# Kernel tuning notes

Measured on AMD Instinct MI355X. Metric: run time of the kernel, lower is better.

Reference implementation:

```python
import jax, jax.numpy as jnp
import numpy as np

N, E = 200_000, 1_000_000
WIDTH, NUM_HEAD = 128, 8
WN, WA = 1, 1            # width_norm, width_act
C = WIDTH * WN           # pre/norm channels
A = WIDTH * WA           # gate/value channels
BOND_SIZE, BAG = 33, 3
EPS = 1e-5               # GroupNorm eps (torch default)


def group_norm(x, groups, eps=EPS):
    # x: [E, C]; normalize per sample per group (affine=False, spatial size 1)
    e, c = x.shape
    xg = x.reshape(e, groups, c // groups)
    m = xg.mean(-1, keepdims=True)
    v = ((xg - m) ** 2).mean(-1, keepdims=True)
    return ((xg - m) * jax.lax.rsqrt(v + eps)).reshape(e, c)


def grouped1x1(x, w, groups):
    # grouped Conv1d with kernel 1, no bias. x: [E, Cin], w: [Cout, Cin//groups]
    e, cin = x.shape
    cout = w.shape[0]
    xg = x.reshape(e, groups, cin // groups)
    wg = w.reshape(groups, cout // groups, cin // groups)
    return jnp.einsum('egi,goi->ego', xg, wg).reshape(e, cout)


def setup_inputs() -> dict:
    key = jax.random.key(0)
    ks = jax.random.split(key, 12)
    x = jax.random.normal(ks[0], (N, WIDTH), jnp.float32)
    # degrees clamped to >= 1 in the original model
    deg = jnp.floor(jax.random.uniform(ks[1], (N,), jnp.float32, 1.0, 8.0))
    edge_idx = jax.random.randint(ks[2], (2, E), 0, N)
    edge_attr = jax.random.randint(ks[3], (E, BAG), 0, BOND_SIZE)
    s_in = 1.0 / np.sqrt(WIDTH)
    s_g = 1.0 / np.sqrt(C // NUM_HEAD)
    s_p = 1.0 / np.sqrt(A)
    pre0_w = jax.random.normal(ks[4], (C, WIDTH), jnp.float32) * s_in
    pre0_b = jnp.zeros((C,), jnp.float32)
    pre1_w = jax.random.normal(ks[5], (C, WIDTH), jnp.float32) * s_in
    pre1_b = jnp.zeros((C,), jnp.float32)
    emb = jax.random.normal(ks[6], (BOND_SIZE, C), jnp.float32)
    emb = emb.at[0].set(0.0)  # padding_idx=0
    gate_w = jax.random.normal(ks[7], (A, C // NUM_HEAD), jnp.float32) * s_g
    value_w = jax.random.normal(ks[8], (A, C // NUM_HEAD), jnp.float32) * s_g
    post_w = jax.random.normal(ks[9], (WIDTH, A), jnp.float32) * s_p
    post_b = jnp.zeros((WIDTH,), jnp.float32)
    degree_param = jnp.full((WIDTH,), -0.01, jnp.float32)
    return {"x": x, "deg": deg, "edge_idx": edge_idx, "edge_attr": edge_attr,
            "pre0_w": pre0_w, "pre0_b": pre0_b, "pre1_w": pre1_w, "pre1_b": pre1_b,
            "emb": emb, "gate_w": gate_w, "value_w": value_w,
            "post_w": post_w, "post_b": post_b, "degree_param": degree_param}


def reference(x, deg, edge_idx, edge_attr, pre0_w, pre0_b, pre1_w, pre1_b,
              emb, gate_w, value_w, post_w, post_b, degree_param):
    n = x.shape[0]
    # conv1x1 projections on nodes, then gather to edges
    h0 = x @ pre0_w.T + pre0_b                      # [N, C]
    h1 = x @ pre1_w.T + pre1_b                      # [N, C]
    xx = h0[edge_idx[0]] + h1[edge_idx[1]]          # [E, C]
    xx = group_norm(xx, NUM_HEAD)
    # EmbeddingBag mean with padding_idx=0 excluded from the mean
    mask = (edge_attr != 0)                          # [E, BAG]
    bag = (emb[edge_attr] * mask[..., None]).sum(1)  # [E, C]
    cnt = jnp.maximum(mask.sum(-1), 1).astype(xx.dtype)
    bag = bag / cnt[:, None]
    # GLU-style gate * value (Dropout is identity at eval)
    gate = jax.nn.relu(grouped1x1(xx + bag, gate_w, NUM_HEAD))  # [E, A]
    val = grouped1x1(xx, value_w, NUM_HEAD)                     # [E, A]
    xx = gate * val
    # scatter-sum back to destination nodes
    agg = jax.ops.segment_sum(xx, edge_idx[1], num_segments=n)  # [N, A]
    out = agg @ post_w.T + post_b                                # [N, WIDTH]
    out = jnp.power(deg[:, None], degree_param) * out
    return out
```

## Files before the change

kernel.cpp:

```cpp
#include <hip/hip_runtime.h>
#include <hip/hip_bf16.h>
#include <hip/hip_fp16.h>


typedef unsigned short u16;
typedef unsigned int   u32;

#define WIDTH 128

#define OFF_W0   0
#define OFF_B0   16384
#define OFF_W1   16512
#define OFF_B1   32896
#define OFF_EMB  33024
#define OFF_GW   37248
#define OFF_VW   39296
#define OFF_PW   41344
#define OFF_PB   57728
#define OFF_DP   57856
#define OFF_DEG  57984
#define ARENA_PAD 258048

typedef __attribute__((ext_vector_type(8))) short bf16x8;
typedef __attribute__((ext_vector_type(4))) float f32x4;
typedef __attribute__((ext_vector_type(2))) __fp16 f16x2;

__device__ __forceinline__ float bfl(u32 p){ return __uint_as_float(p << 16); }
__device__ __forceinline__ float bfh(u32 p){ return __uint_as_float(p & 0xffff0000u); }
__device__ __forceinline__ float b2f(u16 u){ return __uint_as_float(((u32)u) << 16); }
__device__ __forceinline__ u16   f2b(float f){
  u32 u = __float_as_uint(f);
  u += 0x7fffu + ((u >> 16) & 1u);
  return (u16)(u >> 16);
}
__device__ __forceinline__ u16   f2h(float f){ return __half_as_ushort(__float2half(f)); }

__device__ __forceinline__ f16x2 u2h(u32 u){ union { u32 a; f16x2 b; } c; c.a = u; return c.b; }
__device__ __forceinline__ u32   h2u(f16x2 h){ union { f16x2 b; u32 a; } c; c.b = h; return c.a; }

__device__ __forceinline__ float dot2h(f16x2 a, f16x2 b, float c){
#if __has_builtin(__builtin_amdgcn_fdot2)
  return __builtin_amdgcn_fdot2(a, b, c, false);
#else
  return fmaf((float)a.x, (float)b.x, fmaf((float)a.y, (float)b.y, c));
#endif
}

#define SWZF(v, imm) __uint_as_float((u32)__builtin_amdgcn_ds_swizzle((int)__float_as_uint(v), (imm)))

__device__ __forceinline__ bool is_fp32(const void* degsrc){
  return ((*(const u32*)degsrc) & 0xffffu) == 0u;
}

__device__ __forceinline__ bf16x8 cvt8(float4 a, float4 b){
  bf16x8 r;
  r[0]=(short)f2b(a.x); r[1]=(short)f2b(a.y); r[2]=(short)f2b(a.z); r[3]=(short)f2b(a.w);
  r[4]=(short)f2b(b.x); r[5]=(short)f2b(b.y); r[6]=(short)f2b(b.z); r[7]=(short)f2b(b.w);
  return r;
}

__device__ __forceinline__ u16 cvt_one(const void* src, int j, bool f32){
  return f32 ? f2b(((const float*)src)[j]) : ((const u16*)src)[j];
}
__device__ __forceinline__ u16 cvt_one_h(const void* src, int j, bool f32){
  return f32 ? f2h(((const float*)src)[j]) : f2h(b2f(((const u16*)src)[j]));
}

__global__ void k_convert(const void* w0, const void* b0, const void* w1, const void* b1,
                          const void* emb, const void* gw, const void* vw,
                          const void* pw, const void* pb, const void* dp,
                          const void* degsrc, u16* __restrict__ pb16, int total)
{
  const int i = blockIdx.x * 256 + threadIdx.x;
  if (i >= total) return;
  const bool f32 = is_fp32(degsrc);
  u16 v;
  if      (i < OFF_B0 ) v = cvt_one(w0,  i,           f32);
  else if (i < OFF_W1 ) v = cvt_one(b0,  i - OFF_B0,  f32);
  else if (i < OFF_B1 ) v = cvt_one(w1,  i - OFF_W1,  f32);
  else if (i < OFF_EMB) v = cvt_one(b1,  i - OFF_B1,  f32);
  else if (i < OFF_GW ) v = cvt_one(emb, i - OFF_EMB, f32);
  else if (i < OFF_VW ) v = cvt_one_h(gw, i - OFF_GW, f32);
  else if (i < OFF_PW ) v = cvt_one_h(vw, i - OFF_VW, f32);
  else if (i < OFF_PB ) v = cvt_one(pw,  i - OFF_PW,  f32);
  else if (i < OFF_DP ) v = cvt_one(pb,  i - OFF_PB,  f32);
  else if (i < OFF_DEG) v = cvt_one(dp,  i - OFF_DP,  f32);
  else                  v = cvt_one(degsrc, i - OFF_DEG, f32);
  pb16[i] = v;
}

__device__ __forceinline__ float read_f(const void* src, int j, bool f32){
  return f32 ? ((const float*)src)[j] : b2f(((const u16*)src)[j]);
}

__global__ void k_gemb(const void* gwsrc, const void* embsrc, const void* degsrc,
                       float* __restrict__ gemb)
{
  const int tid = blockIdx.x * 256 + threadIdx.x;
  if (tid >= 33 * 128) return;
  const bool f32 = is_fp32(degsrc);
  const int a = tid >> 7, c = tid & 127, g = c >> 4;
  float s = 0.f;
  #pragma unroll
  for (int i = 0; i < 16; ++i)
    s += read_f(gwsrc, c * 16 + i, f32) * read_f(embsrc, a * WIDTH + g * 16 + i, f32);
  gemb[tid] = s;
}

__global__ void k_zero(int* __restrict__ cnt, int n){
  const int i = blockIdx.x * 256 + threadIdx.x;
  if (i < n) cnt[i] = 0;
}

__global__ void k_hist(const int* __restrict__ eidx, int* __restrict__ cnt, int E){
  const int e = blockIdx.x * 256 + threadIdx.x;
  if (e < E) atomicAdd(&cnt[eidx[E + e]], 1);
}

__global__ void k_scan1(const int* __restrict__ cnt, int* __restrict__ bsum, int n){
  const int t = threadIdx.x, b = blockIdx.x;
  const int i0 = b * 1024 + t * 4;
  int s = 0;
  #pragma unroll
  for (int j = 0; j < 4; ++j) { int i = i0 + j; if (i < n) s += cnt[i]; }
  __shared__ int sb[256];
  sb[t] = s; __syncthreads();
  for (int d = 128; d > 0; d >>= 1) { if (t < d) sb[t] += sb[t + d]; __syncthreads(); }
  if (t == 0) bsum[b] = sb[0];
}

__global__ void k_scan2(int* __restrict__ bsum, int nblk){
  const int t = threadIdx.x;
  int v[4];
  const int i0 = t * 4;
  #pragma unroll
  for (int j = 0; j < 4; ++j) { int i = i0 + j; v[j] = (i < nblk) ? bsum[i] : 0; }
  int tsum = v[0] + v[1] + v[2] + v[3];
  __shared__ int sb[256];
  sb[t] = tsum; __syncthreads();
  for (int d = 1; d < 256; d <<= 1) {
    int x = (t >= d) ? sb[t - d] : 0;
    __syncthreads();
    sb[t] += x;
    __syncthreads();
  }
  int run = sb[t] - tsum;
  #pragma unroll
  for (int j = 0; j < 4; ++j) { int nv = run; run += v[j]; v[j] = nv; }
  #pragma unroll
  for (int j = 0; j < 4; ++j) { int i = i0 + j; if (i < nblk) bsum[i] = v[j]; }
}

__global__ void k_scan3(const int* __restrict__ cnt, const int* __restrict__ bsum,
                        int* __restrict__ off, int n){
  const int t = threadIdx.x, b = blockIdx.x;
  const int i0 = b * 1024 + t * 4;
  int c[4];
  #pragma unroll
  for (int j = 0; j < 4; ++j) { int i = i0 + j; c[j] = (i < n) ? cnt[i] : 0; }
  int tsum = c[0] + c[1] + c[2] + c[3];
  __shared__ int sb[256];
  sb[t] = tsum; __syncthreads();
  for (int d = 1; d < 256; d <<= 1) {
    int x = (t >= d) ? sb[t - d] : 0;
    __syncthreads();
    sb[t] += x;
    __syncthreads();
  }
  int run = bsum[b] + sb[t] - tsum;
  #pragma unroll
  for (int j = 0; j < 4; ++j) {
    int i = i0 + j;
    if (i < n) off[i] = run;
    run += c[j];
  }
}

__global__ void k_scatter(const int* __restrict__ eidx, const int* __restrict__ eattr,
                          int* __restrict__ off, u32* __restrict__ ssrc,
                          u32* __restrict__ sattr, int E){
  const int e = blockIdx.x * 256 + threadIdx.x;
  if (e >= E) return;
  const int dst = eidx[E + e];
  const int pos = atomicAdd(&off[dst], 1);
  ssrc[pos] = (u32)eidx[e];
  const u32 a0 = (u32)eattr[e*3+0], a1 = (u32)eattr[e*3+1], a2 = (u32)eattr[e*3+2];
  sattr[pos] = a0 | (a1 << 6) | (a2 << 12);
}

__global__ __launch_bounds__(256, 2) void k_pre(
    const void* __restrict__ x, const u16* __restrict__ pb16,
    u16* __restrict__ h0, u16* __restrict__ h1, const void* __restrict__ degsrc)
{
  const int t = threadIdx.x;
  const int lane = t & 63, lid = lane & 15, quad = lane >> 4;
  const int w = t >> 6, mat = w >> 1, c0 = (w & 1) * 64;
  const int node0 = blockIdx.x * 64;

  const u16* wm = pb16 + (mat ? OFF_W1 : OFF_W0);
  const u16* bs = pb16 + (mat ? OFF_B1 : OFF_B0);
  u16* hout = mat ? h1 : h0;
  const bool f32 = is_fp32(degsrc);

  f32x4 acc[4][4];
  #pragma unroll
  for (int nt = 0; nt < 4; ++nt) {
    const float bias = b2f(bs[c0 + nt * 16 + lid]);
    #pragma unroll
    for (int mt = 0; mt < 4; ++mt)
      #pragma unroll
      for (int r = 0; r < 4; ++r) acc[mt][nt][r] = bias;
  }

  #pragma unroll
  for (int ks = 0; ks < 4; ++ks) {
    bf16x8 a[4], b[4];
    #pragma unroll
    for (int nt = 0; nt < 4; ++nt)
      b[nt] = *(const bf16x8*)(wm + (size_t)(c0 + nt * 16 + lid) * WIDTH + ks * 32 + quad * 8);
    if (f32) {
      #pragma unroll
      for (int mt = 0; mt < 4; ++mt) {
        const float4* xr = (const float4*)((const float*)x +
            (size_t)(node0 + mt * 16 + lid) * WIDTH + ks * 32 + quad * 8);
        a[mt] = cvt8(xr[0], xr[1]);
      }
    } else {
      #pragma unroll
      for (int mt = 0; mt < 4; ++mt)
        a[mt] = *(const bf16x8*)((const u16*)x +
            (size_t)(node0 + mt * 16 + lid) * WIDTH + ks * 32 + quad * 8);
    }
    #pragma unroll
    for (int mt = 0; mt < 4; ++mt)
      #pragma unroll
      for (int nt = 0; nt < 4; ++nt)
        acc[mt][nt] = __builtin_amdgcn_mfma_f32_16x16x32_bf16(a[mt], b[nt], acc[mt][nt], 0, 0, 0);
  }

  #pragma unroll
  for (int mt = 0; mt < 4; ++mt)
    #pragma unroll
    for (int nt = 0; nt < 4; ++nt)
      #pragma unroll
      for (int r = 0; r < 4; ++r)
        hout[(size_t)(node0 + mt * 16 + quad * 4 + r) * WIDTH + c0 + nt * 16 + lid] =
            f2h(acc[mt][nt][r]);
}

__global__ __launch_bounds__(256, 4) void k_agg(
    const u16* __restrict__ h0, const u16* __restrict__ h1,
    const u32* __restrict__ ssrc, const u32* __restrict__ sattr,
    const int* __restrict__ off, const u16* __restrict__ pb16,
    const float* __restrict__ gemb, float* __restrict__ agg, const int N)
{
  const int dst = (blockIdx.x * 256 + threadIdx.x) >> 6;
  if (dst >= N) return;
  const int q = threadIdx.x & 63;
  const int c0 = 2 * q;

  u32 gw0[8], gw1[8], vw0[8], vw1[8];
  {
    const u32* g = (const u32*)(pb16 + OFF_GW + (size_t)c0 * 16);
    const u32* v = (const u32*)(pb16 + OFF_VW + (size_t)c0 * 16);
    #pragma unroll
    for (int i = 0; i < 8; ++i) {
      gw0[i] = g[i]; gw1[i] = g[8 + i];
      vw0[i] = v[i]; vw1[i] = v[8 + i];
    }
  }

  const f16x2 h1h  = u2h(*(const u32*)(h1 + (size_t)dst * WIDTH + c0));
  const f16x2 ones = u2h(0x3C003C00u);

  const int n0 = dst ? off[dst - 1] : 0;
  const int n1 = off[dst];

  float acc0 = 0.f, acc1 = 0.f;

  u32 apw = 0, hp = 0;
  if (n0 < n1) {
    const u32 s0 = ssrc[n0];
    apw = sattr[n0];
    hp  = *(const u32*)(h0 + (size_t)s0 * WIDTH + c0);
  }

  for (int i = n0; i < n1; ++i) {
    const u32 apw_c = apw, hp_c = hp;
    if (i + 1 < n1) {
      const u32 s2 = ssrc[i + 1];
      apw = sattr[i + 1];
      hp  = *(const u32*)(h0 + (size_t)s2 * WIDTH + c0);
    }

    const f16x2 xh = u2h(hp_c) + h1h;

    float s  = dot2h(xh, ones, 0.f);
    float ss = dot2h(xh, xh,   0.f);
    s  += SWZF(s,  0x041F); s  += SWZF(s,  0x081F); s  += SWZF(s,  0x101F);
    ss += SWZF(ss, 0x041F); ss += SWZF(ss, 0x081F); ss += SWZF(ss, 0x101F);
    const float mean = s * 0.0625f;
    const float var  = fmaf(ss, 0.0625f, -mean * mean);
    const float rs   = __builtin_amdgcn_rsqf(var + 1e-5f);
    const float mrs  = mean * rs;
    const float x0 = (float)xh.x, x1 = (float)xh.y;
    const f16x2 xn = __builtin_amdgcn_cvt_pkrtz(fmaf(x0, rs, -mrs), fmaf(x1, rs, -mrs));
    const u32 xnu = h2u(xn);

    const int a0 = apw_c & 63, a1 = (apw_c >> 6) & 63, a2 = (apw_c >> 12) & 63;
    const float2 g0 = *(const float2*)(gemb + (size_t)a0 * WIDTH + c0);
    const float2 g1 = *(const float2*)(gemb + (size_t)a1 * WIDTH + c0);
    const float2 g2 = *(const float2*)(gemb + (size_t)a2 * WIDTH + c0);
    const int cb = (a0 != 0) + (a1 != 0) + (a2 != 0);
    const float inv = __builtin_amdgcn_rcpf((float)(cb | (cb == 0)));

    float ga0 = (g0.x + g1.x + g2.x) * inv;
    float ga1 = (g0.y + g1.y + g2.y) * inv;
    float va0 = 0.f, va1 = 0.f;

#define CSTEP(J) {                                                             \
    const f16x2 xj = u2h((u32)__builtin_amdgcn_ds_swizzle(                     \
        (int)xnu, 0x18 | ((J) << 5)));                                         \
    ga0 = dot2h(xj, u2h(gw0[J]), ga0);                                         \
    ga1 = dot2h(xj, u2h(gw1[J]), ga1);                                         \
    va0 = dot2h(xj, u2h(vw0[J]), va0);                                         \
    va1 = dot2h(xj, u2h(vw1[J]), va1); }
    CSTEP(0) CSTEP(1) CSTEP(2) CSTEP(3) CSTEP(4) CSTEP(5) CSTEP(6) CSTEP(7)
#undef CSTEP

    acc0 = fmaf(fmaxf(ga0, 0.f), va0, acc0);
    acc1 = fmaf(fmaxf(ga1, 0.f), va1, acc1);
  }
  *(float2*)(agg + (size_t)dst * WIDTH + c0) = make_float2(acc0, acc1);
}

__global__ __launch_bounds__(256, 2) void k_post(
    const float* __restrict__ agg, const u16* __restrict__ pb16,
    void* __restrict__ out, const void* __restrict__ degsrc)
{
  const int t = threadIdx.x;
  const int lane = t & 63, lid = lane & 15, quad = lane >> 4;
  const int w = t >> 6, c0 = (w & 1) * 64, mh = (w >> 1) * 32;
  const int node0 = blockIdx.x * 64;
  const bool f32o = is_fp32(degsrc);

  f32x4 acc[2][4];
  float dpc[4];
  #pragma unroll
  for (int nt = 0; nt < 4; ++nt) {
    const float bias = b2f(pb16[OFF_PB + c0 + nt * 16 + lid]);
    dpc[nt] = b2f(pb16[OFF_DP + c0 + nt * 16 + lid]);
    #pragma unroll
    for (int mt = 0; mt < 2; ++mt)
      #pragma unroll
      for (int r = 0; r < 4; ++r) acc[mt][nt][r] = bias;
  }

  #pragma unroll
  for (int ks = 0; ks < 4; ++ks) {
    bf16x8 a[2], b[4];
    #pragma unroll
    for (int nt = 0; nt < 4; ++nt)
      b[nt] = *(const bf16x8*)(pb16 + OFF_PW + (size_t)(c0 + nt * 16 + lid) * WIDTH + ks * 32 + quad * 8);
    #pragma unroll
    for (int mt = 0; mt < 2; ++mt) {
      const float4* ar = (const float4*)(agg +
          (size_t)(node0 + mh + mt * 16 + lid) * WIDTH + ks * 32 + quad * 8);
      a[mt] = cvt8(ar[0], ar[1]);
    }
    #pragma unroll
    for (int mt = 0; mt < 2; ++mt)
      #pragma unroll
      for (int nt = 0; nt < 4; ++nt)
        acc[mt][nt] = __builtin_amdgcn_mfma_f32_16x16x32_bf16(a[mt], b[nt], acc[mt][nt], 0, 0, 0);
  }

  float logd[2][4];
  #pragma unroll
  for (int mt = 0; mt < 2; ++mt)
    #pragma unroll
    for (int r = 0; r < 4; ++r)
      logd[mt][r] = __logf(b2f(pb16[OFF_DEG + node0 + mh + mt * 16 + quad * 4 + r]));

  #pragma unroll
  for (int mt = 0; mt < 2; ++mt)
    #pragma unroll
    for (int nt = 0; nt < 4; ++nt)
      #pragma unroll
      for (int r = 0; r < 4; ++r) {
        const int node = node0 + mh + mt * 16 + quad * 4 + r;
        const float v = acc[mt][nt][r] * __expf(dpc[nt] * logd[mt][r]);
        if (f32o) ((float*)out)[(size_t)node * WIDTH + c0 + nt * 16 + lid] = v;
        else      ((u16*)out)[(size_t)node * WIDTH + c0 + nt * 16 + lid] = f2b(v);
      }
}

extern "C" void kernel_launch(void* const* d_in, const int* in_sizes, int n_in,
                              void* d_out, int out_size, void* d_ws, size_t ws_size,
                              hipStream_t stream)
{
  (void)n_in; (void)out_size; (void)ws_size;
  const void* x     = d_in[0];
  const void* deg   = d_in[1];
  const int*  eidx  = (const int*)d_in[2];
  const int*  eattr = (const int*)d_in[3];

  const int N = in_sizes[1];
  const int E = in_sizes[2] / 2;

  float* agg  = (float*)d_ws;
  u16*   h1   = (u16*)(agg + (size_t)N * WIDTH);
  u16*   pb16 = h1 + (size_t)N * WIDTH;
  float* gemb = (float*)(pb16 + ARENA_PAD);
  int*   cnt  = (int*)(gemb + 33 * WIDTH);
  int*   off  = cnt + N;
  int*   bsum = off + N;
  u32*   ssrc = (u32*)(bsum + 1024);
  u32*   sattr= ssrc + E;
  u16*   h0   = (u16*)d_out;

  const int total = OFF_DEG + N;
  k_convert<<<(total + 255) / 256, 256, 0, stream>>>(
      d_in[4], d_in[5], d_in[6], d_in[7], d_in[8], d_in[9], d_in[10],
      d_in[11], d_in[12], d_in[13], deg, pb16, total);
  k_gemb<<<(33 * 128 + 255) / 256, 256, 0, stream>>>(d_in[9], d_in[8], deg, gemb);

  const int nb = N / 64;
  k_pre<<<nb, 256, 0, stream>>>(x, pb16, h0, h1, deg);

  const int nblk = (N + 1023) / 1024;
  k_zero   <<<(N + 255) / 256, 256, 0, stream>>>(cnt, N);
  k_hist   <<<(E + 255) / 256, 256, 0, stream>>>(eidx, cnt, E);
  k_scan1  <<<nblk, 256, 0, stream>>>(cnt, bsum, N);
  k_scan2  <<<1, 256, 0, stream>>>(bsum, nblk);
  k_scan3  <<<nblk, 256, 0, stream>>>(cnt, bsum, off, N);
  k_scatter<<<(E + 255) / 256, 256, 0, stream>>>(eidx, eattr, off, ssrc, sattr, E);

  k_agg<<<(N * 64 + 255) / 256, 256, 0, stream>>>(
      h0, h1, ssrc, sattr, off, pb16, gemb, agg, N);

  k_post<<<nb, 256, 0, stream>>>(agg, pb16, d_out, deg);
}
```

Measured before the change: 688.6 us.

## Fuse setup kernels, pack edge records, fold GroupNorm algebraically, store agg in fp16

```diff
diff --git a/kernel.cpp b/kernel.cpp
--- a/kernel.cpp
+++ b/kernel.cpp
@@ -22,11 +22,10 @@
 #define ARENA_PAD 258048
 
 typedef __attribute__((ext_vector_type(8))) short bf16x8;
+typedef __attribute__((ext_vector_type(8))) _Float16 f16x8;
 typedef __attribute__((ext_vector_type(4))) float f32x4;
 typedef __attribute__((ext_vector_type(2))) __fp16 f16x2;
 
-__device__ __forceinline__ float bfl(u32 p){ return __uint_as_float(p << 16); }
-__device__ __forceinline__ float bfh(u32 p){ return __uint_as_float(p & 0xffff0000u); }
 __device__ __forceinline__ float b2f(u16 u){ return __uint_as_float(((u32)u) << 16); }
 __device__ __forceinline__ u16   f2b(float f){
   u32 u = __float_as_uint(f);
@@ -46,7 +45,10 @@
 #endif
 }
 
-#define SWZF(v, imm) __uint_as_float((u32)__builtin_amdgcn_ds_swizzle((int)__float_as_uint(v), (imm)))
+#define DPPADD(s, ctrl) {                                                  \
+  const float _t = __uint_as_float((u32)__builtin_amdgcn_update_dpp(       \
+      0, (int)__float_as_uint(s), (ctrl), 0xF, 0xF, true));                \
+  (s) += _t; }
 
 __device__ __forceinline__ bool is_fp32(const void* degsrc){
   return ((*(const u32*)degsrc) & 0xffffu) == 0u;
@@ -65,56 +67,134 @@
 __device__ __forceinline__ u16 cvt_one_h(const void* src, int j, bool f32){
   return f32 ? f2h(((const float*)src)[j]) : f2h(b2f(((const u16*)src)[j]));
 }
-
-__global__ void k_convert(const void* w0, const void* b0, const void* w1, const void* b1,
-                          const void* emb, const void* gw, const void* vw,
-                          const void* pw, const void* pb, const void* dp,
-                          const void* degsrc, u16* __restrict__ pb16, int total)
-{
-  const int i = blockIdx.x * 256 + threadIdx.x;
-  if (i >= total) return;
-  const bool f32 = is_fp32(degsrc);
-  u16 v;
-  if      (i < OFF_B0 ) v = cvt_one(w0,  i,           f32);
-  else if (i < OFF_W1 ) v = cvt_one(b0,  i - OFF_B0,  f32);
-  else if (i < OFF_B1 ) v = cvt_one(w1,  i - OFF_W1,  f32);
-  else if (i < OFF_EMB) v = cvt_one(b1,  i - OFF_B1,  f32);
-  else if (i < OFF_GW ) v = cvt_one(emb, i - OFF_EMB, f32);
-  else if (i < OFF_VW ) v = cvt_one_h(gw, i - OFF_GW, f32);
-  else if (i < OFF_PW ) v = cvt_one_h(vw, i - OFF_VW, f32);
-  else if (i < OFF_PB ) v = cvt_one(pw,  i - OFF_PW,  f32);
-  else if (i < OFF_DP ) v = cvt_one(pb,  i - OFF_PB,  f32);
-  else if (i < OFF_DEG) v = cvt_one(dp,  i - OFF_DP,  f32);
-  else                  v = cvt_one(degsrc, i - OFF_DEG, f32);
-  pb16[i] = v;
-}
-
 __device__ __forceinline__ float read_f(const void* src, int j, bool f32){
   return f32 ? ((const float*)src)[j] : b2f(((const u16*)src)[j]);
 }
 
-__global__ void k_gemb(const void* gwsrc, const void* embsrc, const void* degsrc,
-                       float* __restrict__ gemb)
+__global__ void k_init(const void* w0, const void* b0, const void* w1, const void* b1,
+                       const void* emb, const void* gw, const void* vw,
+                       const void* pw, const void* pb, const void* dp,
+                       const void* degsrc, u16* __restrict__ pb16,
+                       u16* __restrict__ gembh, float* __restrict__ gsums,
+                       int* __restrict__ cnt, int N, int total)
 {
-  const int tid = blockIdx.x * 256 + threadIdx.x;
-  if (tid >= 33 * 128) return;
   const bool f32 = is_fp32(degsrc);
-  const int a = tid >> 7, c = tid & 127, g = c >> 4;
-  float s = 0.f;
-  #pragma unroll
-  for (int i = 0; i < 16; ++i)
-    s += read_f(gwsrc, c * 16 + i, f32) * read_f(embsrc, a * WIDTH + g * 16 + i, f32);
-  gemb[tid] = s;
-}
-
-__global__ void k_zero(int* __restrict__ cnt, int n){
-  const int i = blockIdx.x * 256 + threadIdx.x;
-  if (i < n) cnt[i] = 0;
-}
-
-__global__ void k_hist(const int* __restrict__ eidx, int* __restrict__ cnt, int E){
-  const int e = blockIdx.x * 256 + threadIdx.x;
-  if (e < E) atomicAdd(&cnt[eidx[E + e]], 1);
+  const int nbz = (N + 255) >> 8;
+  const int nbc = (total + 255) >> 8;
+  int b = blockIdx.x;
+  const int t = threadIdx.x;
+
+  if (b < nbz) {
+    const int i = b * 256 + t;
+    if (i < N) cnt[i] = 0;
+    return;
+  }
+  b -= nbz;
+  if (b < nbc) {
+    const int i = b * 256 + t;
+    if (i >= total) return;
+    u16 v;
+    if      (i < OFF_B0 ) v = cvt_one(w0,  i,           f32);
+    else if (i < OFF_W1 ) v = cvt_one(b0,  i - OFF_B0,  f32);
+    else if (i < OFF_B1 ) v = cvt_one(w1,  i - OFF_W1,  f32);
+    else if (i < OFF_EMB) v = cvt_one(b1,  i - OFF_B1,  f32);
+    else if (i < OFF_GW ) v = cvt_one(emb, i - OFF_EMB, f32);
+    else if (i < OFF_VW ) v = cvt_one_h(gw, i - OFF_GW, f32);
+    else if (i < OFF_PW ) v = cvt_one_h(vw, i - OFF_VW, f32);
+    else if (i < OFF_PB ) v = cvt_one_h(pw, i - OFF_PW, f32);
+    else if (i < OFF_DP ) v = cvt_one(pb,  i - OFF_PB,  f32);
+    else if (i < OFF_DEG) v = cvt_one(dp,  i - OFF_DP,  f32);
+    else                  v = cvt_one(degsrc, i - OFF_DEG, f32);
+    pb16[i] = v;
+    return;
+  }
+  b -= nbc;
+  if (b < 17) {
+    const int tid = b * 256 + t;
+    if (tid >= 33 * 128) return;
+    const int a = tid >> 7, c = tid & 127, g = c >> 4;
+    float s = 0.f;
+    #pragma unroll
+    for (int i = 0; i < 16; ++i)
+      s += read_f(gw, c * 16 + i, f32) * read_f(emb, a * WIDTH + g * 16 + i, f32);
+    gembh[tid] = f2h(s);
+    return;
+  }
+  if (t < 256) {
+    const int c = t & 127;
+    const void* src = (t >> 7) ? vw : gw;
+    float s = 0.f;
+    #pragma unroll
+    for (int i = 0; i < 16; ++i) s += read_f(src, c * 16 + i, f32);
+    gsums[t] = s;
+  }
+}
+
+__global__ __launch_bounds__(256, 2) void k_pre_hist(
+    const void* __restrict__ x, const u16* __restrict__ pb16,
+    u16* __restrict__ h0, u16* __restrict__ h1, const void* __restrict__ degsrc,
+    const int* __restrict__ eidx, int* __restrict__ cnt, int E, int npre)
+{
+  if ((int)blockIdx.x >= npre) {
+    const int e = ((int)blockIdx.x - npre) * 256 + threadIdx.x;
+    if (e < E) atomicAdd(&cnt[eidx[E + e]], 1);
+    return;
+  }
+
+  const int t = threadIdx.x;
+  const int lane = t & 63, lid = lane & 15, quad = lane >> 4;
+  const int w = t >> 6, mat = w >> 1, c0 = (w & 1) * 64;
+  const int node0 = blockIdx.x * 64;
+
+  const u16* wm = pb16 + (mat ? OFF_W1 : OFF_W0);
+  const u16* bs = pb16 + (mat ? OFF_B1 : OFF_B0);
+  u16* hout = mat ? h1 : h0;
+  const bool f32 = is_fp32(degsrc);
+
+  f32x4 acc[4][4];
+  #pragma unroll
+  for (int nt = 0; nt < 4; ++nt) {
+    const float bias = b2f(bs[c0 + nt * 16 + lid]);
+    #pragma unroll
+    for (int mt = 0; mt < 4; ++mt)
+      #pragma unroll
+      for (int r = 0; r < 4; ++r) acc[mt][nt][r] = bias;
+  }
+
+  #pragma unroll
+  for (int ks = 0; ks < 4; ++ks) {
+    bf16x8 a[4], b[4];
+    #pragma unroll
+    for (int nt = 0; nt < 4; ++nt)
+      b[nt] = *(const bf16x8*)(wm + (size_t)(c0 + nt * 16 + lid) * WIDTH + ks * 32 + quad * 8);
+    if (f32) {
+      #pragma unroll
+      for (int mt = 0; mt < 4; ++mt) {
+        const float4* xr = (const float4*)((const float*)x +
+            (size_t)(node0 + mt * 16 + lid) * WIDTH + ks * 32 + quad * 8);
+        a[mt] = cvt8(xr[0], xr[1]);
+      }
+    } else {
+      #pragma unroll
+      for (int mt = 0; mt < 4; ++mt)
+        a[mt] = *(const bf16x8*)((const u16*)x +
+            (size_t)(node0 + mt * 16 + lid) * WIDTH + ks * 32 + quad * 8);
+    }
+    #pragma unroll
+    for (int mt = 0; mt < 4; ++mt)
+      #pragma unroll
+      for (int nt = 0; nt < 4; ++nt)
+        acc[mt][nt] = __builtin_amdgcn_mfma_f32_16x16x32_bf16(a[mt], b[nt], acc[mt][nt], 0, 0, 0);
+  }
+
+  #pragma unroll
+  for (int mt = 0; mt < 4; ++mt)
+    #pragma unroll
+    for (int nt = 0; nt < 4; ++nt)
+      #pragma unroll
+      for (int r = 0; r < 4; ++r)
+        hout[(size_t)(node0 + mt * 16 + quad * 4 + r) * WIDTH + c0 + nt * 16 + lid] =
+            f2h(acc[mt][nt][r]);
 }
 
 __global__ void k_scan1(const int* __restrict__ cnt, int* __restrict__ bsum, int n){
@@ -177,85 +257,23 @@
 }
 
 __global__ void k_scatter(const int* __restrict__ eidx, const int* __restrict__ eattr,
-                          int* __restrict__ off, u32* __restrict__ ssrc,
-                          u32* __restrict__ sattr, int E){
+                          int* __restrict__ off, uint2* __restrict__ sedge, int E){
   const int e = blockIdx.x * 256 + threadIdx.x;
   if (e >= E) return;
   const int dst = eidx[E + e];
   const int pos = atomicAdd(&off[dst], 1);
-  ssrc[pos] = (u32)eidx[e];
   const u32 a0 = (u32)eattr[e*3+0], a1 = (u32)eattr[e*3+1], a2 = (u32)eattr[e*3+2];
-  sattr[pos] = a0 | (a1 << 6) | (a2 << 12);
-}
-
-__global__ __launch_bounds__(256, 2) void k_pre(
-    const void* __restrict__ x, const u16* __restrict__ pb16,
-    u16* __restrict__ h0, u16* __restrict__ h1, const void* __restrict__ degsrc)
-{
-  const int t = threadIdx.x;
-  const int lane = t & 63, lid = lane & 15, quad = lane >> 4;
-  const int w = t >> 6, mat = w >> 1, c0 = (w & 1) * 64;
-  const int node0 = blockIdx.x * 64;
-
-  const u16* wm = pb16 + (mat ? OFF_W1 : OFF_W0);
-  const u16* bs = pb16 + (mat ? OFF_B1 : OFF_B0);
-  u16* hout = mat ? h1 : h0;
-  const bool f32 = is_fp32(degsrc);
-
-  f32x4 acc[4][4];
-  #pragma unroll
-  for (int nt = 0; nt < 4; ++nt) {
-    const float bias = b2f(bs[c0 + nt * 16 + lid]);
-    #pragma unroll
-    for (int mt = 0; mt < 4; ++mt)
-      #pragma unroll
-      for (int r = 0; r < 4; ++r) acc[mt][nt][r] = bias;
-  }
-
-  #pragma unroll
-  for (int ks = 0; ks < 4; ++ks) {
-    bf16x8 a[4], b[4];
-    #pragma unroll
-    for (int nt = 0; nt < 4; ++nt)
-      b[nt] = *(const bf16x8*)(wm + (size_t)(c0 + nt * 16 + lid) * WIDTH + ks * 32 + quad * 8);
-    if (f32) {
-      #pragma unroll
-      for (int mt = 0; mt < 4; ++mt) {
-        const float4* xr = (const float4*)((const float*)x +
-            (size_t)(node0 + mt * 16 + lid) * WIDTH + ks * 32 + quad * 8);
-        a[mt] = cvt8(xr[0], xr[1]);
-      }
-    } else {
-      #pragma unroll
-      for (int mt = 0; mt < 4; ++mt)
-        a[mt] = *(const bf16x8*)((const u16*)x +
-            (size_t)(node0 + mt * 16 + lid) * WIDTH + ks * 32 + quad * 8);
-    }
-    #pragma unroll
-    for (int mt = 0; mt < 4; ++mt)
-      #pragma unroll
-      for (int nt = 0; nt < 4; ++nt)
-        acc[mt][nt] = __builtin_amdgcn_mfma_f32_16x16x32_bf16(a[mt], b[nt], acc[mt][nt], 0, 0, 0);
-  }
-
-  #pragma unroll
-  for (int mt = 0; mt < 4; ++mt)
-    #pragma unroll
-    for (int nt = 0; nt < 4; ++nt)
-      #pragma unroll
-      for (int r = 0; r < 4; ++r)
-        hout[(size_t)(node0 + mt * 16 + quad * 4 + r) * WIDTH + c0 + nt * 16 + lid] =
-            f2h(acc[mt][nt][r]);
+  sedge[pos] = make_uint2((u32)eidx[e], a0 | (a1 << 6) | (a2 << 12));
 }
 
 __global__ __launch_bounds__(256, 4) void k_agg(
     const u16* __restrict__ h0, const u16* __restrict__ h1,
-    const u32* __restrict__ ssrc, const u32* __restrict__ sattr,
-    const int* __restrict__ off, const u16* __restrict__ pb16,
-    const float* __restrict__ gemb, float* __restrict__ agg, const int N)
+    const uint2* __restrict__ sedge, const int* __restrict__ off,
+    const u16* __restrict__ pb16, const u16* __restrict__ gembh,
+    const float* __restrict__ gsums, u16* __restrict__ aggh, const int N)
 {
-  const int dst = (blockIdx.x * 256 + threadIdx.x) >> 6;
-  if (dst >= N) return;
+  const int base = ((blockIdx.x * 256 + threadIdx.x) >> 6) * 4;
+  if (base >= N) return;
   const int q = threadIdx.x & 63;
   const int c0 = 2 * q;
 
@@ -269,73 +287,97 @@
       vw0[i] = v[i]; vw1[i] = v[8 + i];
     }
   }
-
-  const f16x2 h1h  = u2h(*(const u32*)(h1 + (size_t)dst * WIDTH + c0));
+  const float gs0 = gsums[c0],           gs1 = gsums[c0 + 1];
+  const float nv0 = -gsums[128 + c0],    nv1 = -gsums[128 + c0 + 1];
   const f16x2 ones = u2h(0x3C003C00u);
 
-  const int n0 = dst ? off[dst - 1] : 0;
-  const int n1 = off[dst];
-
-  float acc0 = 0.f, acc1 = 0.f;
-
-  u32 apw = 0, hp = 0;
-  if (n0 < n1) {
-    const u32 s0 = ssrc[n0];
-    apw = sattr[n0];
-    hp  = *(const u32*)(h0 + (size_t)s0 * WIDTH + c0);
-  }
-
-  for (int i = n0; i < n1; ++i) {
-    const u32 apw_c = apw, hp_c = hp;
-    if (i + 1 < n1) {
-      const u32 s2 = ssrc[i + 1];
-      apw = sattr[i + 1];
-      hp  = *(const u32*)(h0 + (size_t)s2 * WIDTH + c0);
+  u32 h1w[4]; int nend[4];
+  #pragma unroll
+  for (int d = 0; d < 4; ++d) {
+    const int dst = min(base + d, N - 1);
+    h1w[d]  = *(const u32*)(h1 + (size_t)dst * WIDTH + c0);
+    nend[d] = off[dst];
+  }
+  int ncur = base ? off[base - 1] : 0;
+  const int nlast = nend[3];
+
+  u32 hp = 0, g0w = 0, g1w = 0, g2w = 0; float pinv = 1.f;
+  if (ncur < nlast) {
+    const uint2 ep = sedge[ncur];
+    hp  = *(const u32*)(h0 + (size_t)ep.x * WIDTH + c0);
+    const int a0 = ep.y & 63, a1 = (ep.y >> 6) & 63, a2 = (ep.y >> 12) & 63;
+    g0w = *(const u32*)(gembh + (size_t)a0 * WIDTH + c0);
+    g1w = *(const u32*)(gembh + (size_t)a1 * WIDTH + c0);
+    g2w = *(const u32*)(gembh + (size_t)a2 * WIDTH + c0);
+    const int cb = (a0 != 0) + (a1 != 0) + (a2 != 0);
+    pinv = __builtin_amdgcn_rcpf((float)(cb | (cb == 0)));
+  }
+
+  #pragma unroll
+  for (int d = 0; d < 4; ++d) {
+    const f16x2 h1h = u2h(h1w[d]);
+    const int n1 = nend[d];
+    float acc0 = 0.f, acc1 = 0.f;
+
+    for (int i = ncur; i < n1; ++i) {
+      const u32 hp_c = hp, g0c = g0w, g1c = g1w, g2c = g2w;
+      const float inv_c = pinv;
+      if (i + 1 < nlast) {
+        const uint2 ep = sedge[i + 1];
+        hp  = *(const u32*)(h0 + (size_t)ep.x * WIDTH + c0);
+        const int a0 = ep.y & 63, a1 = (ep.y >> 6) & 63, a2 = (ep.y >> 12) & 63;
+        g0w = *(const u32*)(gembh + (size_t)a0 * WIDTH + c0);
+        g1w = *(const u32*)(gembh + (size_t)a1 * WIDTH + c0);
+        g2w = *(const u32*)(gembh + (size_t)a2 * WIDTH + c0);
+        const int cb = (a0 != 0) + (a1 != 0) + (a2 != 0);
+        pinv = __builtin_amdgcn_rcpf((float)(cb | (cb == 0)));
+      }
+
+      const f16x2 xh = u2h(hp_c) + h1h;
+      const u32 xu = h2u(xh);
+
+      float s  = dot2h(xh, ones, 0.f);
+      float ss = dot2h(xh, xh,   0.f);
+      DPPADD(s, 0xB1);  DPPADD(ss, 0xB1);
+      DPPADD(s, 0x4E);  DPPADD(ss, 0x4E);
+      DPPADD(s, 0x141); DPPADD(ss, 0x141);
+      const float mean = s * 0.0625f;
+      const float var  = fmaf(ss, 0.0625f, -mean * mean);
+      const float rs   = __builtin_amdgcn_rsqf(var + 1e-5f);
+      const float mrs  = mean * rs;
+
+      float rg0 = 0.f, rg1 = 0.f, rv0 = 0.f, rv1 = 0.f;
+#define CSTEP(J) {                                                             \
+      const f16x2 xj = u2h((u32)__builtin_amdgcn_ds_swizzle(                   \
+          (int)xu, 0x18 | ((J) << 5)));                                        \
+      rg0 = dot2h(xj, u2h(gw0[J]), rg0);                                       \
+      rg1 = dot2h(xj, u2h(gw1[J]), rg1);                                       \
+      rv0 = dot2h(xj, u2h(vw0[J]), rv0);                                       \
+      rv1 = dot2h(xj, u2h(vw1[J]), rv1); }
+      CSTEP(0) CSTEP(1) CSTEP(2) CSTEP(3) CSTEP(4) CSTEP(5) CSTEP(6) CSTEP(7)
+#undef CSTEP
+
+      const f16x2 gsum3 = u2h(g0c) + u2h(g1c) + u2h(g2c);
+      const float bg0 = (float)gsum3.x * inv_c;
+      const float bg1 = (float)gsum3.y * inv_c;
+
+      const float ga0 = fmaf(rs, rg0, fmaf(-mrs, gs0, bg0));
+      const float ga1 = fmaf(rs, rg1, fmaf(-mrs, gs1, bg1));
+      const float va0 = fmaf(rs, rv0, mrs * nv0);
+      const float va1 = fmaf(rs, rv1, mrs * nv1);
+      acc0 = fmaf(fmaxf(ga0, 0.f), va0, acc0);
+      acc1 = fmaf(fmaxf(ga1, 0.f), va1, acc1);
     }
 
-    const f16x2 xh = u2h(hp_c) + h1h;
-
-    float s  = dot2h(xh, ones, 0.f);
-    float ss = dot2h(xh, xh,   0.f);
-    s  += SWZF(s,  0x041F); s  += SWZF(s,  0x081F); s  += SWZF(s,  0x101F);
-    ss += SWZF(ss, 0x041F); ss += SWZF(ss, 0x081F); ss += SWZF(ss, 0x101F);
-    const float mean = s * 0.0625f;
-    const float var  = fmaf(ss, 0.0625f, -mean * mean);
-    const float rs   = __builtin_amdgcn_rsqf(var + 1e-5f);
-    const float mrs  = mean * rs;
-    const float x0 = (float)xh.x, x1 = (float)xh.y;
-    const f16x2 xn = __builtin_amdgcn_cvt_pkrtz(fmaf(x0, rs, -mrs), fmaf(x1, rs, -mrs));
-    const u32 xnu = h2u(xn);
-
-    const int a0 = apw_c & 63, a1 = (apw_c >> 6) & 63, a2 = (apw_c >> 12) & 63;
-    const float2 g0 = *(const float2*)(gemb + (size_t)a0 * WIDTH + c0);
-    const float2 g1 = *(const float2*)(gemb + (size_t)a1 * WIDTH + c0);
-    const float2 g2 = *(const float2*)(gemb + (size_t)a2 * WIDTH + c0);
-    const int cb = (a0 != 0) + (a1 != 0) + (a2 != 0);
-    const float inv = __builtin_amdgcn_rcpf((float)(cb | (cb == 0)));
-
-    float ga0 = (g0.x + g1.x + g2.x) * inv;
-    float ga1 = (g0.y + g1.y + g2.y) * inv;
-    float va0 = 0.f, va1 = 0.f;
-
-#define CSTEP(J) {                                                             \
-    const f16x2 xj = u2h((u32)__builtin_amdgcn_ds_swizzle(                     \
-        (int)xnu, 0x18 | ((J) << 5)));                                         \
-    ga0 = dot2h(xj, u2h(gw0[J]), ga0);                                         \
-    ga1 = dot2h(xj, u2h(gw1[J]), ga1);                                         \
-    va0 = dot2h(xj, u2h(vw0[J]), va0);                                         \
-    va1 = dot2h(xj, u2h(vw1[J]), va1); }
-    CSTEP(0) CSTEP(1) CSTEP(2) CSTEP(3) CSTEP(4) CSTEP(5) CSTEP(6) CSTEP(7)
-#undef CSTEP
-
-    acc0 = fmaf(fmaxf(ga0, 0.f), va0, acc0);
-    acc1 = fmaf(fmaxf(ga1, 0.f), va1, acc1);
-  }
-  *(float2*)(agg + (size_t)dst * WIDTH + c0) = make_float2(acc0, acc1);
+    if (base + d < N)
+      *(u32*)(aggh + (size_t)(base + d) * WIDTH + c0) =
+          h2u(__builtin_amdgcn_cvt_pkrtz(acc0, acc1));
+    ncur = n1;
+  }
 }
 
 __global__ __launch_bounds__(256, 2) void k_post(
-    const float* __restrict__ agg, const u16* __restrict__ pb16,
+    const u16* __restrict__ aggh, const u16* __restrict__ pb16,
     void* __restrict__ out, const void* __restrict__ degsrc)
 {
   const int t = threadIdx.x;
@@ -358,21 +400,19 @@
 
   #pragma unroll
   for (int ks = 0; ks < 4; ++ks) {
-    bf16x8 a[2], b[4];
+    f16x8 a[2], b[4];
     #pragma unroll
     for (int nt = 0; nt < 4; ++nt)
-      b[nt] = *(const bf16x8*)(pb16 + OFF_PW + (size_t)(c0 + nt * 16 + lid) * WIDTH + ks * 32 + quad * 8);
-    #pragma unroll
-    for (int mt = 0; mt < 2; ++mt) {
-      const float4* ar = (const float4*)(agg +
+      b[nt] = *(const f16x8*)(pb16 + OFF_PW + (size_t)(c0 + nt * 16 + lid) * WIDTH + ks * 32 + quad * 8);
+    #pragma unroll
+    for (int mt = 0; mt < 2; ++mt)
+      a[mt] = *(const f16x8*)(aggh +
           (size_t)(node0 + mh + mt * 16 + lid) * WIDTH + ks * 32 + quad * 8);
-      a[mt] = cvt8(ar[0], ar[1]);
-    }
     #pragma unroll
     for (int mt = 0; mt < 2; ++mt)
       #pragma unroll
       for (int nt = 0; nt < 4; ++nt)
-        acc[mt][nt] = __builtin_amdgcn_mfma_f32_16x16x32_bf16(a[mt], b[nt], acc[mt][nt], 0, 0, 0);
+        acc[mt][nt] = __builtin_amdgcn_mfma_f32_16x16x32_f16(a[mt], b[nt], acc[mt][nt], 0, 0, 0);
   }
 
   float logd[2][4];
@@ -408,36 +448,36 @@
   const int N = in_sizes[1];
   const int E = in_sizes[2] / 2;
 
-  float* agg  = (float*)d_ws;
-  u16*   h1   = (u16*)(agg + (size_t)N * WIDTH);
+  u16*   aggh = (u16*)d_ws;
+  u16*   h1   = (u16*)((float*)d_ws + (size_t)N * WIDTH);
   u16*   pb16 = h1 + (size_t)N * WIDTH;
-  float* gemb = (float*)(pb16 + ARENA_PAD);
-  int*   cnt  = (int*)(gemb + 33 * WIDTH);
+  u16*   gembh= pb16 + ARENA_PAD;
+  float* gsums= (float*)(gembh + 33 * WIDTH);
+  int*   cnt  = (int*)(gsums + 256);
   int*   off  = cnt + N;
   int*   bsum = off + N;
-  u32*   ssrc = (u32*)(bsum + 1024);
-  u32*   sattr= ssrc + E;
+  uint2* sedge= (uint2*)(bsum + 1024);
   u16*   h0   = (u16*)d_out;
 
   const int total = OFF_DEG + N;
-  k_convert<<<(total + 255) / 256, 256, 0, stream>>>(
+  const int nbz = (N + 255) / 256;
+  const int nbc = (total + 255) / 256;
+  k_init<<<nbz + nbc + 18, 256, 0, stream>>>(
       d_in[4], d_in[5], d_in[6], d_in[7], d_in[8], d_in[9], d_in[10],
-      d_in[11], d_in[12], d_in[13], deg, pb16, total);
-  k_gemb<<<(33 * 128 + 255) / 256, 256, 0, stream>>>(d_in[9], d_in[8], deg, gemb);
-
-  const int nb = N / 64;
-  k_pre<<<nb, 256, 0, stream>>>(x, pb16, h0, h1, deg);
+      d_in[11], d_in[12], d_in[13], deg, pb16, gembh, gsums, cnt, N, total);
+
+  const int npre = N / 64;
+  const int nbh  = (E + 255) / 256;
+  k_pre_hist<<<npre + nbh, 256, 0, stream>>>(x, pb16, h0, h1, deg, eidx, cnt, E, npre);
 
   const int nblk = (N + 1023) / 1024;
-  k_zero   <<<(N + 255) / 256, 256, 0, stream>>>(cnt, N);
-  k_hist   <<<(E + 255) / 256, 256, 0, stream>>>(eidx, cnt, E);
   k_scan1  <<<nblk, 256, 0, stream>>>(cnt, bsum, N);
   k_scan2  <<<1, 256, 0, stream>>>(bsum, nblk);
   k_scan3  <<<nblk, 256, 0, stream>>>(cnt, bsum, off, N);
-  k_scatter<<<(E + 255) / 256, 256, 0, stream>>>(eidx, eattr, off, ssrc, sattr, E);
-
-  k_agg<<<(N * 64 + 255) / 256, 256, 0, stream>>>(
-      h0, h1, ssrc, sattr, off, pb16, gemb, agg, N);
-
-  k_post<<<nb, 256, 0, stream>>>(agg, pb16, d_out, deg);
-}
+  k_scatter<<<nbh, 256, 0, stream>>>(eidx, eattr, off, sedge, E);
+
+  k_agg<<<((size_t)N * 16 + 255) / 256, 256, 0, stream>>>(
+      h0, h1, sedge, off, pb16, gembh, gsums, aggh, N);
+
+  k_post<<<N / 64, 256, 0, stream>>>(aggh, pb16, d_out, deg);
+}
```

Result: faster. 609.9 us (-11.4%).
